# Performance work log

Measured on AMD Instinct MI355X. Metric: run time of the kernel, lower is better.

The kernel has to match this reference:

```python
import jax, jax.numpy as jnp
import numpy as np

DK = 64  # embedding_size / h = 1024 / 16


def setup_inputs() -> dict:
    key = jax.random.key(0)
    k1, k2, k3 = jax.random.split(key, 3)
    S = 8192
    return {
        "q": jax.random.normal(k1, (S, DK), dtype=jnp.float32),
        "k": jax.random.normal(k2, (S, DK), dtype=jnp.float32),
        "v": jax.random.normal(k3, (S, DK), dtype=jnp.float32),
    }


def reference(q, k, v):
    # scores: [S, S]; NOTE: source scales by 1/dk (not 1/sqrt(dk)) — kept faithful.
    qk = jnp.matmul(q, k.T) * (1.0 / DK)
    S = qk.shape[0]
    # causal mask: position (i, j) allowed iff i >= j (0 added), else -inf
    i = jnp.arange(S)[:, None]
    j = jnp.arange(S)[None, :]
    qk = jnp.where(i >= j, qk, -jnp.inf)
    attn = jax.nn.softmax(qk, axis=-1)
    return jnp.matmul(attn, v)
```

## Files before the change

### kernel.cpp

```cpp
#include <hip/hip_runtime.h>
#include <hip/hip_bf16.h>

#define S_LEN 8192
#define DKD   64
#define BM    32
#define BN    64
#define NW    2
#define PAD   8
#define LDK   (DKD + PAD)
#define LDN   (BN + PAD)

#define CHUNK 1024
#define NC    (S_LEN / CHUNK)

#define WS_NEED ((size_t)3 * S_LEN * DKD * 2 + (size_t)NC * S_LEN * 4 + (size_t)NC * S_LEN * DKD * 2)

typedef __bf16 bf16x8 __attribute__((ext_vector_type(8)));
typedef float  f32x4  __attribute__((ext_vector_type(4)));
typedef unsigned short ushort8v __attribute__((ext_vector_type(8)));
typedef unsigned short ushort4v __attribute__((ext_vector_type(4)));

__device__ __forceinline__ unsigned short f2bf(float f) {
  union { float f; unsigned u; } v; v.f = f;
  unsigned u = v.u;
  unsigned r = (u + 0x7fffu + ((u >> 16) & 1u)) >> 16;
  return (unsigned short)r;
}
__device__ __forceinline__ float bf2f(unsigned short s) {
  union { unsigned u; float f; } v; v.u = ((unsigned)s) << 16;
  return v.f;
}

__global__ __launch_bounds__(256) void conv_qk(const float* __restrict__ q,
                                               const float* __restrict__ k,
                                               unsigned short* __restrict__ Qb,
                                               unsigned short* __restrict__ Kb) {
  int idx = blockIdx.x * 256 + threadIdx.x;
  const float* src = blockIdx.y ? k : q;
  unsigned short* dst = blockIdx.y ? Kb : Qb;
  float sc = blockIdx.y ? 1.0f : (1.0f / 64.0f);
  float4 v = *(const float4*)(src + (size_t)idx * 4);
  ushort4v o = { f2bf(v.x * sc), f2bf(v.y * sc), f2bf(v.z * sc), f2bf(v.w * sc) };
  *(ushort4v*)(dst + (size_t)idx * 4) = o;
}

__global__ __launch_bounds__(256) void conv_vt(const float* __restrict__ v,
                                               unsigned short* __restrict__ Vtb) {
  __shared__ unsigned short Ls[64][72];
  int b = blockIdx.x, tid = threadIdx.x;
#pragma unroll
  for (int j = 0; j < 4; ++j) {
    int vi = tid + j * 256;
    int row = vi >> 4, c4 = vi & 15;
    float4 x = *(const float4*)(v + ((size_t)(b * 64 + row)) * 64 + c4 * 4);
    Ls[row][c4 * 4 + 0] = f2bf(x.x);
    Ls[row][c4 * 4 + 1] = f2bf(x.y);
    Ls[row][c4 * 4 + 2] = f2bf(x.z);
    Ls[row][c4 * 4 + 3] = f2bf(x.w);
  }
  __syncthreads();
#pragma unroll
  for (int j = 0; j < 4; ++j) {
    int ci = tid + j * 256;
    int d = ci >> 4, kq = ci & 15;
    ushort4v o = { Ls[kq * 4 + 0][d], Ls[kq * 4 + 1][d],
                   Ls[kq * 4 + 2][d], Ls[kq * 4 + 3][d] };
    *(ushort4v*)(Vtb + (size_t)d * S_LEN + b * 64 + kq * 4) = o;
  }
}

__global__ __launch_bounds__(128) void attn_partial(const unsigned short* __restrict__ Qb,
                                                    const unsigned short* __restrict__ Kb,
                                                    const unsigned short* __restrict__ Vtb,
                                                    unsigned short* __restrict__ Opart,
                                                    float* __restrict__ l_ws) {
  const int qt = blockIdx.x, cch = blockIdx.y;
  const int q0 = qt * BM, chunk0 = cch * CHUNK;
  if (chunk0 > q0) return;

  __shared__ __align__(16) unsigned short QP[BM][LDK];
  __shared__ __align__(16) unsigned short Ks[BN][LDK];
  __shared__ __align__(16) unsigned short Vts[DKD][LDN];

  const int tid = threadIdx.x, wave = tid >> 6, lane = tid & 63;
  const int col = lane & 15, quad = lane >> 4;
  const int n_kt = min(CHUNK / BN, (q0 + BM - chunk0 + BN - 1) / BN);

#pragma unroll
  for (int j = 0; j < 2; ++j) {
    int vi = tid + j * 128;
    int row = vi >> 3, ch = vi & 7;
    *(ushort8v*)&QP[row][ch * 8] = *(const ushort8v*)(Qb + (size_t)(q0 + row) * DKD + ch * 8);
  }
  ushort8v Kreg[4], Vreg[4];
#pragma unroll
  for (int j = 0; j < 4; ++j) {
    int vi = tid + j * 128;
    int row = vi >> 3, ch = vi & 7;
    Kreg[j] = *(const ushort8v*)(Kb + (size_t)(chunk0 + row) * DKD + ch * 8);
    Vreg[j] = *(const ushort8v*)(Vtb + (size_t)row * S_LEN + chunk0 + ch * 8);
  }
#pragma unroll
  for (int j = 0; j < 4; ++j) {
    int vi = tid + j * 128;
    int row = vi >> 3, ch = vi & 7;
    *(ushort8v*)&Ks[row][ch * 8]  = Kreg[j];
    *(ushort8v*)&Vts[row][ch * 8] = Vreg[j];
  }
  __syncthreads();

  const unsigned short* qrow = &QP[wave * 16 + col][0];
  bf16x8 a0 = *(const bf16x8*)(qrow + quad * 8);
  bf16x8 a1 = *(const bf16x8*)(qrow + 32 + quad * 8);

  float lpart[4] = {0.0f, 0.0f, 0.0f, 0.0f};
  f32x4 Of[4];
#pragma unroll
  for (int i = 0; i < 4; ++i) Of[i] = f32x4{0.0f, 0.0f, 0.0f, 0.0f};

  for (int it = 0; it < n_kt; ++it) {
    const int k0 = chunk0 + it * BN;
    const bool pf = (it + 1 < n_kt);

    if (pf) {
      const int k0n = k0 + BN;
#pragma unroll
      for (int j = 0; j < 4; ++j) {
        int vi = tid + j * 128;
        int row = vi >> 3, ch = vi & 7;
        Kreg[j] = *(const ushort8v*)(Kb + (size_t)(k0n + row) * DKD + ch * 8);
        Vreg[j] = *(const ushort8v*)(Vtb + (size_t)row * S_LEN + k0n + ch * 8);
      }
    }

    f32x4 Sf[4];
#pragma unroll
    for (int t = 0; t < 4; ++t) {
      f32x4 acc = f32x4{0.0f, 0.0f, 0.0f, 0.0f};
      acc = __builtin_amdgcn_mfma_f32_16x16x32_bf16(a0, *(const bf16x8*)(&Ks[t * 16 + col][quad * 8]), acc, 0, 0, 0);
      acc = __builtin_amdgcn_mfma_f32_16x16x32_bf16(a1, *(const bf16x8*)(&Ks[t * 16 + col][32 + quad * 8]), acc, 0, 0, 0);
      Sf[t] = acc;
    }

    const int qb = q0 + wave * 16 + quad * 4;
#pragma unroll
    for (int t = 0; t < 4; ++t) {
      int kidx = k0 + t * 16 + col;
#pragma unroll
      for (int r = 0; r < 4; ++r) {
        float p = __expf(Sf[t][r]);
        p = (kidx <= qb + r) ? p : 0.0f;
        Sf[t][r] = p;
        lpart[r] += p;
      }
    }

#pragma unroll
    for (int t = 0; t < 4; ++t)
#pragma unroll
      for (int r = 0; r < 4; ++r)
        QP[wave * 16 + quad * 4 + r][t * 16 + col] = f2bf(Sf[t][r]);

    const unsigned short* prow = &QP[wave * 16 + col][0];
#pragma unroll
    for (int dt = 0; dt < 4; ++dt) {
#pragma unroll
      for (int c = 0; c < 2; ++c) {
        bf16x8 a = *(const bf16x8*)(prow + c * 32 + quad * 8);
        bf16x8 b = *(const bf16x8*)(&Vts[dt * 16 + col][c * 32 + quad * 8]);
        Of[dt] = __builtin_amdgcn_mfma_f32_16x16x32_bf16(a, b, Of[dt], 0, 0, 0);
      }
    }

    if (pf) {
      __syncthreads();
#pragma unroll
      for (int j = 0; j < 4; ++j) {
        int vi = tid + j * 128;
        int row = vi >> 3, ch = vi & 7;
        *(ushort8v*)&Ks[row][ch * 8]  = Kreg[j];
        *(ushort8v*)&Vts[row][ch * 8] = Vreg[j];
      }
      __syncthreads();
    }
  }

#pragma unroll
  for (int off = 1; off <= 8; off <<= 1)
#pragma unroll
    for (int r = 0; r < 4; ++r)
      lpart[r] += __shfl_xor(lpart[r], off);

#pragma unroll
  for (int r = 0; r < 4; ++r) {
    int rowg = q0 + wave * 16 + quad * 4 + r;
    if (col == 0) l_ws[cch * S_LEN + rowg] = lpart[r];
#pragma unroll
    for (int dt = 0; dt < 4; ++dt)
      Opart[((size_t)cch * S_LEN + rowg) * DKD + dt * 16 + col] = f2bf(Of[dt][r]);
  }
}

__global__ __launch_bounds__(256) void attn_merge(const unsigned short* __restrict__ Opart,
                                                  const float* __restrict__ l_ws,
                                                  float* __restrict__ out) {
  int idx = blockIdx.x * 256 + threadIdx.x;
  int row = idx >> 6, colm = idx & 63;
  int nc = (row >> 10) + 1;
  float L = 0.0f, acc = 0.0f;
  for (int c = 0; c < nc; ++c) {
    L   += l_ws[c * S_LEN + row];
    acc += bf2f(Opart[((size_t)c * S_LEN + row) * DKD + colm]);
  }
  out[idx] = acc / L;
}

__global__ __launch_bounds__(128) void attn_fwd(const float* __restrict__ qg,
                                                const float* __restrict__ kg,
                                                const float* __restrict__ vg,
                                                float* __restrict__ out) {
  __shared__ __align__(16) unsigned short Qs[BM][LDK];
  __shared__ __align__(16) unsigned short Ksh[BN][LDK];
  __shared__ __align__(16) unsigned short Vt[DKD][LDN];
  __shared__ __align__(16) unsigned short Ps[NW][16][LDN];

  const int tid = threadIdx.x, wave = tid >> 6, lane = tid & 63;
  const int col = lane & 15, quad = lane >> 4;
  const int q0 = blockIdx.x * BM;

#pragma unroll
  for (int r = 0; r < (BM * DKD / 4) / 128; ++r) {
    int vi = tid + r * 128;
    int row = vi >> 4, c4 = vi & 15;
    float4 val = *(const float4*)(qg + (q0 + row) * DKD + c4 * 4);
    Qs[row][c4 * 4 + 0] = f2bf(val.x);
    Qs[row][c4 * 4 + 1] = f2bf(val.y);
    Qs[row][c4 * 4 + 2] = f2bf(val.z);
    Qs[row][c4 * 4 + 3] = f2bf(val.w);
  }

  float m_run[4], l_run[4];
  f32x4 Of[4];
#pragma unroll
  for (int i = 0; i < 4; ++i) {
    m_run[i] = -1e30f; l_run[i] = 0.0f;
    Of[i] = f32x4{0.0f, 0.0f, 0.0f, 0.0f};
  }

  const int n_tiles = (q0 + BM - 1) / BN + 1;
  for (int it = 0; it < n_tiles; ++it) {
    __syncthreads();
    const int k0 = it * BN;
#pragma unroll
    for (int r = 0; r < (BN * DKD / 4) / 128; ++r) {
      int vi = tid + r * 128;
      int row = vi >> 4, c4 = vi & 15;
      float4 kv = *(const float4*)(kg + (k0 + row) * DKD + c4 * 4);
      Ksh[row][c4 * 4 + 0] = f2bf(kv.x);
      Ksh[row][c4 * 4 + 1] = f2bf(kv.y);
      Ksh[row][c4 * 4 + 2] = f2bf(kv.z);
      Ksh[row][c4 * 4 + 3] = f2bf(kv.w);
      float4 vv = *(const float4*)(vg + (k0 + row) * DKD + c4 * 4);
      Vt[c4 * 4 + 0][row] = f2bf(vv.x);
      Vt[c4 * 4 + 1][row] = f2bf(vv.y);
      Vt[c4 * 4 + 2][row] = f2bf(vv.z);
      Vt[c4 * 4 + 3][row] = f2bf(vv.w);
    }
    __syncthreads();

    f32x4 Sf[4];
    const unsigned short* qrow = &Qs[wave * 16 + col][0];
#pragma unroll
    for (int t = 0; t < 4; ++t) {
      f32x4 acc = f32x4{0.0f, 0.0f, 0.0f, 0.0f};
#pragma unroll
      for (int c = 0; c < 2; ++c) {
        bf16x8 a = *(const bf16x8*)(qrow + c * 32 + quad * 8);
        bf16x8 b = *(const bf16x8*)(&Ksh[t * 16 + col][c * 32 + quad * 8]);
        acc = __builtin_amdgcn_mfma_f32_16x16x32_bf16(a, b, acc, 0, 0, 0);
      }
      Sf[t] = acc;
    }

    const float scale = 1.0f / 64.0f;
    float rmax[4] = {-1e30f, -1e30f, -1e30f, -1e30f};
#pragma unroll
    for (int t = 0; t < 4; ++t) {
      int kidx = k0 + t * 16 + col;
#pragma unroll
      for (int r = 0; r < 4; ++r) {
        int qidx = q0 + wave * 16 + quad * 4 + r;
        float s = Sf[t][r] * scale;
        s = (kidx <= qidx) ? s : -1e30f;
        Sf[t][r] = s;
        rmax[r] = fmaxf(rmax[r], s);
      }
    }
#pragma unroll
    for (int off = 1; off <= 8; off <<= 1)
#pragma unroll
      for (int r = 0; r < 4; ++r)
        rmax[r] = fmaxf(rmax[r], __shfl_xor(rmax[r], off));

    float alpha[4], rsum[4];
#pragma unroll
    for (int r = 0; r < 4; ++r) {
      float mn = fmaxf(m_run[r], rmax[r]);
      alpha[r] = __expf(m_run[r] - mn);
      m_run[r] = mn;
      rsum[r] = 0.0f;
    }
#pragma unroll
    for (int t = 0; t < 4; ++t)
#pragma unroll
      for (int r = 0; r < 4; ++r) {
        float p = __expf(Sf[t][r] - m_run[r]);
        Sf[t][r] = p;
        rsum[r] += p;
      }
#pragma unroll
    for (int off = 1; off <= 8; off <<= 1)
#pragma unroll
      for (int r = 0; r < 4; ++r)
        rsum[r] += __shfl_xor(rsum[r], off);
#pragma unroll
    for (int r = 0; r < 4; ++r)
      l_run[r] = l_run[r] * alpha[r] + rsum[r];
#pragma unroll
    for (int dt = 0; dt < 4; ++dt)
#pragma unroll
      for (int r = 0; r < 4; ++r)
        Of[dt][r] *= alpha[r];

#pragma unroll
    for (int t = 0; t < 4; ++t)
#pragma unroll
      for (int r = 0; r < 4; ++r)
        Ps[wave][quad * 4 + r][t * 16 + col] = f2bf(Sf[t][r]);
    __syncthreads();

    const unsigned short* prow = &Ps[wave][col][0];
#pragma unroll
    for (int dt = 0; dt < 4; ++dt) {
#pragma unroll
      for (int c = 0; c < 2; ++c) {
        bf16x8 a = *(const bf16x8*)(prow + c * 32 + quad * 8);
        bf16x8 b = *(const bf16x8*)(&Vt[dt * 16 + col][c * 32 + quad * 8]);
        Of[dt] = __builtin_amdgcn_mfma_f32_16x16x32_bf16(a, b, Of[dt], 0, 0, 0);
      }
    }
  }

#pragma unroll
  for (int r = 0; r < 4; ++r) {
    float inv = 1.0f / l_run[r];
    int qrow_g = q0 + wave * 16 + quad * 4 + r;
#pragma unroll
    for (int dt = 0; dt < 4; ++dt)
      out[qrow_g * DKD + dt * 16 + col] = Of[dt][r] * inv;
  }
}

extern "C" void kernel_launch(void* const* d_in, const int* in_sizes, int n_in,
                              void* d_out, int out_size, void* d_ws, size_t ws_size,
                              hipStream_t stream) {
  const float* q = (const float*)d_in[0];
  const float* k = (const float*)d_in[1];
  const float* v = (const float*)d_in[2];
  float* out = (float*)d_out;

  if (ws_size >= WS_NEED) {
    unsigned short* Qb  = (unsigned short*)d_ws;
    unsigned short* Kb  = Qb + (size_t)S_LEN * DKD;
    unsigned short* Vtb = Kb + (size_t)S_LEN * DKD;
    float* l_ws         = (float*)(Vtb + (size_t)S_LEN * DKD);
    unsigned short* Opart = (unsigned short*)(l_ws + (size_t)NC * S_LEN);

    hipLaunchKernelGGL(conv_qk, dim3(S_LEN * DKD / 1024, 2), dim3(256), 0, stream, q, k, Qb, Kb);
    hipLaunchKernelGGL(conv_vt, dim3(S_LEN / 64), dim3(256), 0, stream, v, Vtb);
    hipLaunchKernelGGL(attn_partial, dim3(S_LEN / BM, NC), dim3(128), 0, stream,
                       Qb, Kb, Vtb, Opart, l_ws);
    hipLaunchKernelGGL(attn_merge, dim3(S_LEN * DKD / 256), dim3(256), 0, stream,
                       Opart, l_ws, out);
  } else {
    hipLaunchKernelGGL(attn_fwd, dim3(S_LEN / BM), dim3(128), 0, stream, q, k, v, out);
  }
}
```

Before: 101.4 us.

## Fuse Q conversion into attention, merge prep kernels, permute layouts for packed stores

The separate Q and K conversion kernels and the V-transpose kernel are folded into one precompute launch. Q is now read as fp32 and converted straight into MFMA register fragments inside the attention kernel. The partial kernel moves to 64-row query tiles with four waves, which doubles the reuse of each K/V tile loaded into shared memory. The V-transpose and the P/O layouts use a permuted column order, so P and the partial outputs can be written as packed 8-byte stores and the merge kernel can do vector loads and stores. This trades an extra launch and the Q workspace for more complex indexing. The packed conversion rounds half-up instead of to-nearest-even, and the larger tiles leave fewer blocks in flight.

```diff
diff --git a/kernel.cpp b/kernel.cpp
--- a/kernel.cpp
+++ b/kernel.cpp
@@ -3,17 +3,15 @@
 
 #define S_LEN 8192
 #define DKD   64
-#define BM    32
+#define BM    64
 #define BN    64
-#define NW    2
 #define PAD   8
 #define LDK   (DKD + PAD)
-#define LDN   (BN + PAD)
 
 #define CHUNK 1024
 #define NC    (S_LEN / CHUNK)
 
-#define WS_NEED ((size_t)3 * S_LEN * DKD * 2 + (size_t)NC * S_LEN * 4 + (size_t)NC * S_LEN * DKD * 2)
+#define WS_NEED ((size_t)2 * S_LEN * DKD * 2 + (size_t)NC * S_LEN * 4 + (size_t)NC * S_LEN * DKD * 2)
 
 typedef __bf16 bf16x8 __attribute__((ext_vector_type(8)));
 typedef float  f32x4  __attribute__((ext_vector_type(4)));
@@ -23,53 +21,65 @@
 __device__ __forceinline__ unsigned short f2bf(float f) {
   union { float f; unsigned u; } v; v.f = f;
   unsigned u = v.u;
-  unsigned r = (u + 0x7fffu + ((u >> 16) & 1u)) >> 16;
-  return (unsigned short)r;
+  return (unsigned short)((u + 0x7fffu + ((u >> 16) & 1u)) >> 16);
 }
 __device__ __forceinline__ float bf2f(unsigned short s) {
   union { unsigned u; float f; } v; v.u = ((unsigned)s) << 16;
   return v.f;
 }
-
-__global__ __launch_bounds__(256) void conv_qk(const float* __restrict__ q,
-                                               const float* __restrict__ k,
-                                               unsigned short* __restrict__ Qb,
-                                               unsigned short* __restrict__ Kb) {
-  int idx = blockIdx.x * 256 + threadIdx.x;
-  const float* src = blockIdx.y ? k : q;
-  unsigned short* dst = blockIdx.y ? Kb : Qb;
-  float sc = blockIdx.y ? 1.0f : (1.0f / 64.0f);
-  float4 v = *(const float4*)(src + (size_t)idx * 4);
-  ushort4v o = { f2bf(v.x * sc), f2bf(v.y * sc), f2bf(v.z * sc), f2bf(v.w * sc) };
-  *(ushort4v*)(dst + (size_t)idx * 4) = o;
-}
-
-__global__ __launch_bounds__(256) void conv_vt(const float* __restrict__ v,
-                                               unsigned short* __restrict__ Vtb) {
+__device__ __forceinline__ unsigned pk2(float a, float b) {
+  union { float f; unsigned u; } x, y; x.f = a; y.f = b;
+  return ((x.u + 0x8000u) >> 16) | ((y.u + 0x8000u) & 0xffff0000u);
+}
+__device__ __forceinline__ bf16x8 q_frag8(const float* p, float sc) {
+  float4 u = *(const float4*)p;
+  float4 w = *(const float4*)(p + 4);
+  union { ushort8v s; bf16x8 b; } r;
+  r.s[0] = f2bf(u.x * sc); r.s[1] = f2bf(u.y * sc);
+  r.s[2] = f2bf(u.z * sc); r.s[3] = f2bf(u.w * sc);
+  r.s[4] = f2bf(w.x * sc); r.s[5] = f2bf(w.y * sc);
+  r.s[6] = f2bf(w.z * sc); r.s[7] = f2bf(w.w * sc);
+  return r.b;
+}
+
+__global__ __launch_bounds__(256) void precompute(const float* __restrict__ k,
+                                                  const float* __restrict__ v,
+                                                  unsigned short* __restrict__ Kb,
+                                                  unsigned short* __restrict__ Vtb) {
   __shared__ unsigned short Ls[64][72];
-  int b = blockIdx.x, tid = threadIdx.x;
-#pragma unroll
-  for (int j = 0; j < 4; ++j) {
-    int vi = tid + j * 256;
-    int row = vi >> 4, c4 = vi & 15;
-    float4 x = *(const float4*)(v + ((size_t)(b * 64 + row)) * 64 + c4 * 4);
-    Ls[row][c4 * 4 + 0] = f2bf(x.x);
-    Ls[row][c4 * 4 + 1] = f2bf(x.y);
-    Ls[row][c4 * 4 + 2] = f2bf(x.z);
-    Ls[row][c4 * 4 + 3] = f2bf(x.w);
-  }
-  __syncthreads();
-#pragma unroll
-  for (int j = 0; j < 4; ++j) {
-    int ci = tid + j * 256;
-    int d = ci >> 4, kq = ci & 15;
-    ushort4v o = { Ls[kq * 4 + 0][d], Ls[kq * 4 + 1][d],
-                   Ls[kq * 4 + 2][d], Ls[kq * 4 + 3][d] };
-    *(ushort4v*)(Vtb + (size_t)d * S_LEN + b * 64 + kq * 4) = o;
-  }
-}
-
-__global__ __launch_bounds__(128) void attn_partial(const unsigned short* __restrict__ Qb,
+  const int b = blockIdx.x, tid = threadIdx.x;
+  if (blockIdx.y == 0) {
+    size_t base = (size_t)b * 64 * DKD;
+#pragma unroll
+    for (int j = 0; j < 4; ++j) {
+      int vi = tid + j * 256;
+      float4 x = *(const float4*)(k + base + (size_t)vi * 4);
+      ushort4v o = { f2bf(x.x), f2bf(x.y), f2bf(x.z), f2bf(x.w) };
+      *(ushort4v*)(Kb + base + (size_t)vi * 4) = o;
+    }
+  } else {
+#pragma unroll
+    for (int j = 0; j < 4; ++j) {
+      int vi = tid + j * 256;
+      int row = vi >> 4, c4 = vi & 15;
+      float4 x = *(const float4*)(v + ((size_t)(b * 64 + row)) * DKD + c4 * 4);
+      Ls[row][c4 * 4 + 0] = f2bf(x.x);
+      Ls[row][c4 * 4 + 1] = f2bf(x.y);
+      Ls[row][c4 * 4 + 2] = f2bf(x.z);
+      Ls[row][c4 * 4 + 3] = f2bf(x.w);
+    }
+    __syncthreads();
+#pragma unroll
+    for (int j = 0; j < 4; ++j) {
+      int ci = tid + j * 256;
+      int d = ci >> 4, c0 = ci & 15;
+      ushort4v o = { Ls[c0][d], Ls[c0 + 16][d], Ls[c0 + 32][d], Ls[c0 + 48][d] };
+      *(ushort4v*)(Vtb + (size_t)d * S_LEN + b * 64 + c0 * 4) = o;
+    }
+  }
+}
+
+__global__ __launch_bounds__(256) void attn_partial(const float* __restrict__ qg,
                                                     const unsigned short* __restrict__ Kb,
                                                     const unsigned short* __restrict__ Vtb,
                                                     unsigned short* __restrict__ Opart,
@@ -80,44 +90,30 @@
 
   __shared__ __align__(16) unsigned short QP[BM][LDK];
   __shared__ __align__(16) unsigned short Ks[BN][LDK];
-  __shared__ __align__(16) unsigned short Vts[DKD][LDN];
+  __shared__ __align__(16) unsigned short Vts[DKD][LDK];
 
   const int tid = threadIdx.x, wave = tid >> 6, lane = tid & 63;
   const int col = lane & 15, quad = lane >> 4;
-  const int n_kt = min(CHUNK / BN, (q0 + BM - chunk0 + BN - 1) / BN);
+  const int n_kt = min(CHUNK / BN, ((q0 - chunk0) >> 6) + 1);
+
+  const float* qp = qg + (size_t)(q0 + wave * 16 + col) * DKD;
+  bf16x8 a0 = q_frag8(qp + quad * 8, 1.0f / 64.0f);
+  bf16x8 a1 = q_frag8(qp + 32 + quad * 8, 1.0f / 64.0f);
 
 #pragma unroll
   for (int j = 0; j < 2; ++j) {
-    int vi = tid + j * 128;
-    int row = vi >> 3, ch = vi & 7;
-    *(ushort8v*)&QP[row][ch * 8] = *(const ushort8v*)(Qb + (size_t)(q0 + row) * DKD + ch * 8);
-  }
-  ushort8v Kreg[4], Vreg[4];
-#pragma unroll
-  for (int j = 0; j < 4; ++j) {
-    int vi = tid + j * 128;
-    int row = vi >> 3, ch = vi & 7;
-    Kreg[j] = *(const ushort8v*)(Kb + (size_t)(chunk0 + row) * DKD + ch * 8);
-    Vreg[j] = *(const ushort8v*)(Vtb + (size_t)row * S_LEN + chunk0 + ch * 8);
-  }
-#pragma unroll
-  for (int j = 0; j < 4; ++j) {
-    int vi = tid + j * 128;
-    int row = vi >> 3, ch = vi & 7;
-    *(ushort8v*)&Ks[row][ch * 8]  = Kreg[j];
-    *(ushort8v*)&Vts[row][ch * 8] = Vreg[j];
+    int vi = tid + j * 256, row = vi >> 3, ch = vi & 7;
+    *(ushort8v*)&Ks[row][ch * 8]  = *(const ushort8v*)(Kb + ((size_t)(chunk0 + row)) * DKD + ch * 8);
+    *(ushort8v*)&Vts[row][ch * 8] = *(const ushort8v*)(Vtb + (size_t)row * S_LEN + chunk0 + ch * 8);
   }
   __syncthreads();
-
-  const unsigned short* qrow = &QP[wave * 16 + col][0];
-  bf16x8 a0 = *(const bf16x8*)(qrow + quad * 8);
-  bf16x8 a1 = *(const bf16x8*)(qrow + 32 + quad * 8);
 
   float lpart[4] = {0.0f, 0.0f, 0.0f, 0.0f};
   f32x4 Of[4];
 #pragma unroll
   for (int i = 0; i < 4; ++i) Of[i] = f32x4{0.0f, 0.0f, 0.0f, 0.0f};
 
+  ushort8v Kreg[2], Vreg[2];
   for (int it = 0; it < n_kt; ++it) {
     const int k0 = chunk0 + it * BN;
     const bool pf = (it + 1 < n_kt);
@@ -125,10 +121,9 @@
     if (pf) {
       const int k0n = k0 + BN;
 #pragma unroll
-      for (int j = 0; j < 4; ++j) {
-        int vi = tid + j * 128;
-        int row = vi >> 3, ch = vi & 7;
-        Kreg[j] = *(const ushort8v*)(Kb + (size_t)(k0n + row) * DKD + ch * 8);
+      for (int j = 0; j < 2; ++j) {
+        int vi = tid + j * 256, row = vi >> 3, ch = vi & 7;
+        Kreg[j] = *(const ushort8v*)(Kb + ((size_t)(k0n + row)) * DKD + ch * 8);
         Vreg[j] = *(const ushort8v*)(Vtb + (size_t)row * S_LEN + k0n + ch * 8);
       }
     }
@@ -156,28 +151,27 @@
     }
 
 #pragma unroll
-    for (int t = 0; t < 4; ++t)
-#pragma unroll
-      for (int r = 0; r < 4; ++r)
-        QP[wave * 16 + quad * 4 + r][t * 16 + col] = f2bf(Sf[t][r]);
+    for (int r = 0; r < 4; ++r) {
+      uint2 w2;
+      w2.x = pk2(Sf[0][r], Sf[1][r]);
+      w2.y = pk2(Sf[2][r], Sf[3][r]);
+      *(uint2*)&QP[wave * 16 + quad * 4 + r][col * 4] = w2;
+    }
 
     const unsigned short* prow = &QP[wave * 16 + col][0];
+    bf16x8 pa0 = *(const bf16x8*)(prow + quad * 8);
+    bf16x8 pa1 = *(const bf16x8*)(prow + 32 + quad * 8);
 #pragma unroll
     for (int dt = 0; dt < 4; ++dt) {
-#pragma unroll
-      for (int c = 0; c < 2; ++c) {
-        bf16x8 a = *(const bf16x8*)(prow + c * 32 + quad * 8);
-        bf16x8 b = *(const bf16x8*)(&Vts[dt * 16 + col][c * 32 + quad * 8]);
-        Of[dt] = __builtin_amdgcn_mfma_f32_16x16x32_bf16(a, b, Of[dt], 0, 0, 0);
-      }
+      Of[dt] = __builtin_amdgcn_mfma_f32_16x16x32_bf16(pa0, *(const bf16x8*)(&Vts[dt * 16 + col][quad * 8]), Of[dt], 0, 0, 0);
+      Of[dt] = __builtin_amdgcn_mfma_f32_16x16x32_bf16(pa1, *(const bf16x8*)(&Vts[dt * 16 + col][32 + quad * 8]), Of[dt], 0, 0, 0);
     }
 
     if (pf) {
       __syncthreads();
 #pragma unroll
-      for (int j = 0; j < 4; ++j) {
-        int vi = tid + j * 128;
-        int row = vi >> 3, ch = vi & 7;
+      for (int j = 0; j < 2; ++j) {
+        int vi = tid + j * 256, row = vi >> 3, ch = vi & 7;
         *(ushort8v*)&Ks[row][ch * 8]  = Kreg[j];
         *(ushort8v*)&Vts[row][ch * 8] = Vreg[j];
       }
@@ -195,9 +189,10 @@
   for (int r = 0; r < 4; ++r) {
     int rowg = q0 + wave * 16 + quad * 4 + r;
     if (col == 0) l_ws[cch * S_LEN + rowg] = lpart[r];
-#pragma unroll
-    for (int dt = 0; dt < 4; ++dt)
-      Opart[((size_t)cch * S_LEN + rowg) * DKD + dt * 16 + col] = f2bf(Of[dt][r]);
+    uint2 o2;
+    o2.x = pk2(Of[0][r], Of[1][r]);
+    o2.y = pk2(Of[2][r], Of[3][r]);
+    *(uint2*)(Opart + ((size_t)cch * S_LEN + rowg) * DKD + col * 4) = o2;
   }
 }
 
@@ -205,38 +200,49 @@
                                                   const float* __restrict__ l_ws,
                                                   float* __restrict__ out) {
   int idx = blockIdx.x * 256 + threadIdx.x;
-  int row = idx >> 6, colm = idx & 63;
+  int row = idx >> 3, m = idx & 7;
   int nc = (row >> 10) + 1;
-  float L = 0.0f, acc = 0.0f;
+
+  float acc[8] = {0, 0, 0, 0, 0, 0, 0, 0};
+  float L = 0.0f;
   for (int c = 0; c < nc; ++c) {
-    L   += l_ws[c * S_LEN + row];
-    acc += bf2f(Opart[((size_t)c * S_LEN + row) * DKD + colm]);
-  }
-  out[idx] = acc / L;
+    L += l_ws[c * S_LEN + row];
+    ushort8v o = *(const ushort8v*)(Opart + ((size_t)c * S_LEN + row) * DKD + m * 8);
+#pragma unroll
+    for (int j = 0; j < 8; ++j) acc[j] += bf2f(o[j]);
+  }
+  float inv = 1.0f / L;
+#pragma unroll
+  for (int j0 = 0; j0 < 4; ++j0) {
+    float2 w = { acc[j0] * inv, acc[j0 + 4] * inv };
+    *(float2*)(out + (size_t)row * DKD + 16 * j0 + 2 * m) = w;
+  }
 }
 
 __global__ __launch_bounds__(128) void attn_fwd(const float* __restrict__ qg,
                                                 const float* __restrict__ kg,
                                                 const float* __restrict__ vg,
                                                 float* __restrict__ out) {
-  __shared__ __align__(16) unsigned short Qs[BM][LDK];
+  __shared__ __align__(16) unsigned short Qs[32][LDK];
   __shared__ __align__(16) unsigned short Ksh[BN][LDK];
-  __shared__ __align__(16) unsigned short Vt[DKD][LDN];
-  __shared__ __align__(16) unsigned short Ps[NW][16][LDN];
+  __shared__ __align__(16) unsigned short Vt[DKD][LDK];
+  __shared__ __align__(16) unsigned short Ps[2][16][LDK];
 
   const int tid = threadIdx.x, wave = tid >> 6, lane = tid & 63;
   const int col = lane & 15, quad = lane >> 4;
-  const int q0 = blockIdx.x * BM;
-
-#pragma unroll
-  for (int r = 0; r < (BM * DKD / 4) / 128; ++r) {
+  const int q0 = blockIdx.x * 32;
+
+#pragma unroll
+  for (int r = 0; r < 4; ++r) {
     int vi = tid + r * 128;
     int row = vi >> 4, c4 = vi & 15;
-    float4 val = *(const float4*)(qg + (q0 + row) * DKD + c4 * 4);
-    Qs[row][c4 * 4 + 0] = f2bf(val.x);
-    Qs[row][c4 * 4 + 1] = f2bf(val.y);
-    Qs[row][c4 * 4 + 2] = f2bf(val.z);
-    Qs[row][c4 * 4 + 3] = f2bf(val.w);
+    if (row < 32) {
+      float4 val = *(const float4*)(qg + (size_t)(q0 + row) * DKD + c4 * 4);
+      Qs[row][c4 * 4 + 0] = f2bf(val.x);
+      Qs[row][c4 * 4 + 1] = f2bf(val.y);
+      Qs[row][c4 * 4 + 2] = f2bf(val.z);
+      Qs[row][c4 * 4 + 3] = f2bf(val.w);
+    }
   }
 
   float m_run[4], l_run[4];
@@ -247,20 +253,20 @@
     Of[i] = f32x4{0.0f, 0.0f, 0.0f, 0.0f};
   }
 
-  const int n_tiles = (q0 + BM - 1) / BN + 1;
+  const int n_tiles = (q0 + 32 - 1) / BN + 1;
   for (int it = 0; it < n_tiles; ++it) {
     __syncthreads();
     const int k0 = it * BN;
 #pragma unroll
-    for (int r = 0; r < (BN * DKD / 4) / 128; ++r) {
+    for (int r = 0; r < 8; ++r) {
       int vi = tid + r * 128;
       int row = vi >> 4, c4 = vi & 15;
-      float4 kv = *(const float4*)(kg + (k0 + row) * DKD + c4 * 4);
+      float4 kv = *(const float4*)(kg + (size_t)(k0 + row) * DKD + c4 * 4);
       Ksh[row][c4 * 4 + 0] = f2bf(kv.x);
       Ksh[row][c4 * 4 + 1] = f2bf(kv.y);
       Ksh[row][c4 * 4 + 2] = f2bf(kv.z);
       Ksh[row][c4 * 4 + 3] = f2bf(kv.w);
-      float4 vv = *(const float4*)(vg + (k0 + row) * DKD + c4 * 4);
+      float4 vv = *(const float4*)(vg + (size_t)(k0 + row) * DKD + c4 * 4);
       Vt[c4 * 4 + 0][row] = f2bf(vv.x);
       Vt[c4 * 4 + 1][row] = f2bf(vv.y);
       Vt[c4 * 4 + 2][row] = f2bf(vv.z);
@@ -357,7 +363,7 @@
     int qrow_g = q0 + wave * 16 + quad * 4 + r;
 #pragma unroll
     for (int dt = 0; dt < 4; ++dt)
-      out[qrow_g * DKD + dt * 16 + col] = Of[dt][r] * inv;
+      out[(size_t)qrow_g * DKD + dt * 16 + col] = Of[dt][r] * inv;
   }
 }
 
@@ -370,19 +376,17 @@
   float* out = (float*)d_out;
 
   if (ws_size >= WS_NEED) {
-    unsigned short* Qb  = (unsigned short*)d_ws;
-    unsigned short* Kb  = Qb + (size_t)S_LEN * DKD;
+    unsigned short* Kb  = (unsigned short*)d_ws;
     unsigned short* Vtb = Kb + (size_t)S_LEN * DKD;
     float* l_ws         = (float*)(Vtb + (size_t)S_LEN * DKD);
     unsigned short* Opart = (unsigned short*)(l_ws + (size_t)NC * S_LEN);
 
-    hipLaunchKernelGGL(conv_qk, dim3(S_LEN * DKD / 1024, 2), dim3(256), 0, stream, q, k, Qb, Kb);
-    hipLaunchKernelGGL(conv_vt, dim3(S_LEN / 64), dim3(256), 0, stream, v, Vtb);
-    hipLaunchKernelGGL(attn_partial, dim3(S_LEN / BM, NC), dim3(128), 0, stream,
-                       Qb, Kb, Vtb, Opart, l_ws);
-    hipLaunchKernelGGL(attn_merge, dim3(S_LEN * DKD / 256), dim3(256), 0, stream,
+    hipLaunchKernelGGL(precompute, dim3(S_LEN / 64, 2), dim3(256), 0, stream, k, v, Kb, Vtb);
+    hipLaunchKernelGGL(attn_partial, dim3(S_LEN / BM, NC), dim3(256), 0, stream,
+                       q, Kb, Vtb, Opart, l_ws);
+    hipLaunchKernelGGL(attn_merge, dim3(S_LEN * 8 / 256), dim3(256), 0, stream,
                        Opart, l_ws, out);
   } else {
-    hipLaunchKernelGGL(attn_fwd, dim3(S_LEN / BM), dim3(128), 0, stream, q, k, v, out);
-  }
-}
+    hipLaunchKernelGGL(attn_fwd, dim3(S_LEN / 32), dim3(128), 0, stream, q, k, v, out);
+  }
+}
```

Result: no change. 100.1 us (-1.3%).
